# Performance work log

Hardware: AMD Instinct MI355X
Metric: run time of the kernel (lower is better)

The kernel has to match this reference:

```python
import jax, jax.numpy as jnp
import numpy as np

D = 64      # n_embd (== head_size in this module)
H = 8       # n_heads
B = 4
T = 2048    # seq len == block_size
EPS = 1e-5


def layernorm(x, g, b):
    mu = jnp.mean(x, axis=-1, keepdims=True)
    var = jnp.mean(jnp.square(x - mu), axis=-1, keepdims=True)
    return (x - mu) * jax.lax.rsqrt(var + EPS) * g + b


def setup_inputs() -> dict:
    key = jax.random.key(0)
    ks = jax.random.split(key, 16)
    s = 1.0 / np.sqrt(D)
    inp = {
        'inputs': jax.random.normal(ks[0], (B, T, D), jnp.float32),
        # per-head QKV linears: weight [H, D, D] (in, out), bias [H, D]
        'Wq': jax.random.uniform(ks[1], (H, D, D), jnp.float32, -s, s),
        'bq': jax.random.uniform(ks[2], (H, D), jnp.float32, -s, s),
        'Wk': jax.random.uniform(ks[3], (H, D, D), jnp.float32, -s, s),
        'bk': jax.random.uniform(ks[4], (H, D), jnp.float32, -s, s),
        'Wv': jax.random.uniform(ks[5], (H, D, D), jnp.float32, -s, s),
        'bv': jax.random.uniform(ks[6], (H, D), jnp.float32, -s, s),
        # projection: Linear(H*D -> D)
        'Wp': jax.random.uniform(ks[7], (H * D, D), jnp.float32, -1/np.sqrt(H*D), 1/np.sqrt(H*D)),
        'bp': jax.random.uniform(ks[8], (D,), jnp.float32, -1/np.sqrt(H*D), 1/np.sqrt(H*D)),
        # FFN: D -> 4D -> D
        'W1': jax.random.uniform(ks[9], (D, 4 * D), jnp.float32, -s, s),
        'b1': jax.random.uniform(ks[10], (4 * D,), jnp.float32, -s, s),
        'W2': jax.random.uniform(ks[11], (4 * D, D), jnp.float32, -1/np.sqrt(4*D), 1/np.sqrt(4*D)),
        'b2': jax.random.uniform(ks[12], (D,), jnp.float32, -1/np.sqrt(4*D), 1/np.sqrt(4*D)),
        'g1': jnp.ones((D,), jnp.float32), 'be1': jnp.zeros((D,), jnp.float32),
        'g2': jnp.ones((D,), jnp.float32), 'be2': jnp.zeros((D,), jnp.float32),
    }
    return inp


def reference(inputs, Wq, bq, Wk, bk, Wv, bv, Wp, bp, W1, b1, W2, b2, g1, be1, g2, be2):
    x = inputs
    # per-head full-width QKV: [H, B, T, D]
    q = jnp.einsum('btd,hde->hbte', x, Wq) + bq[:, None, None, :]
    k = jnp.einsum('btd,hde->hbte', x, Wk) + bk[:, None, None, :]
    v = jnp.einsum('btd,hde->hbte', x, Wv) + bv[:, None, None, :]
    # unscaled scores (module has no 1/sqrt(d) scaling)
    scores = jnp.einsum('hbte,hbse->hbts', q, k)  # [H, B, T, T]
    causal = jnp.tril(jnp.ones((T, T), bool))
    scores = jnp.where(causal, scores, -jnp.inf)
    attn = jax.nn.softmax(scores, axis=-1)
    out = jnp.einsum('hbts,hbse->hbte', attn, v)  # [H, B, T, D]
    # torch.cat over heads along last dim -> [B, T, H*D]
    cat = jnp.transpose(out, (1, 2, 0, 3)).reshape(B, T, H * D)
    attn_out = cat @ Wp + bp
    h1 = layernorm(x + attn_out, g1, be1)
    ffn = jax.nn.relu(h1 @ W1 + b1) @ W2 + b2
    return layernorm(h1 + ffn, g2, be2)
```

## Files before the change

### kernel.cpp

```cpp
#include <hip/hip_runtime.h>
#include <hip/hip_bf16.h>
#include <stdint.h>

#define Dd 64
#define Hh 8
#define Bb 4
#define Tt 2048
#define NT (Bb * Tt)

typedef __attribute__((ext_vector_type(4))) float f32x4;
typedef __attribute__((ext_vector_type(8))) __bf16 bf16x8;
typedef __attribute__((ext_vector_type(8))) uint16_t u16x8;
typedef __attribute__((ext_vector_type(4))) uint16_t u16x4;

__device__ __forceinline__ uint16_t f2bf_fast(float f) {
    union { __bf16 h; uint16_t u; } c; c.h = (__bf16)f; return c.u;
}
__device__ __forceinline__ uint32_t pkbf(float a, float b) {
    return (uint32_t)f2bf_fast(a) | ((uint32_t)f2bf_fast(b) << 16);
}

#define SWZ(row, k)   ((row) * 72  + ((k) ^ ((((row) >> 3) & 7) << 3)))
#define PSZ(q, k)     ((q)  * 72  + ((k) ^ ((((q)  >> 2) & 3) << 3)))
#define HSZ(q, k)     ((q)  * 264 + ((k) ^ ((((q)  >> 2) & 3) << 3)))
#define W2SWZ(col, k) ((col) * 264 + ((k) ^ ((((col) >> 3) & 7) << 3)))
#define WPSWZ(col, k) ((col) * 520 + ((k) ^ ((((col) >> 3) & 7) << 3)))

__global__ __launch_bounds__(256) void setup_kernel(
    const float* __restrict__ x,
    const float* __restrict__ Wq, const float* __restrict__ Wk,
    const float* __restrict__ Wv, const float* __restrict__ Wp,
    const float* __restrict__ W1, const float* __restrict__ W2,
    uint16_t* __restrict__ xb, uint16_t* __restrict__ WtAll,
    uint16_t* __restrict__ WptS, uint16_t* __restrict__ W1g,
    uint16_t* __restrict__ W2g)
{
    const int bid = blockIdx.x, t = threadIdx.x;
    if (bid < 256) {
        size_t base = ((size_t)bid * 256 + t) * 8;
        f32x4 a = *(const f32x4*)&x[base];
        f32x4 b = *(const f32x4*)&x[base + 4];
        u16x8 o;
#pragma unroll
        for (int j = 0; j < 4; ++j) { o[j] = f2bf_fast(a[j]); o[4 + j] = f2bf_fast(b[j]); }
        *(u16x8*)&xb[base] = o;
    } else if (bid < 280) {
        const int mh = bid - 256, m = mh / 8, h = mh % 8;
        const float* W = (m == 0) ? Wq : (m == 1) ? Wk : Wv;
        uint16_t* dst = WtAll + (size_t)mh * 4608;
#pragma unroll
        for (int p = 0; p < 4; ++p) {
            int idx = p * 256 + t;
            int k = idx >> 4, c4 = (idx & 15) * 4;
            f32x4 wv = *(const f32x4*)&W[(size_t)(h * 64 + k) * 64 + c4];
#pragma unroll
            for (int j = 0; j < 4; ++j) dst[SWZ(c4 + j, k)] = f2bf_fast(wv[j]);
        }
    } else if (bid < 288) {
        const int j = bid - 280;
#pragma unroll
        for (int p = 0; p < 16; ++p) {
            int idx = p * 256 + t;
            int col = idx & 63, k = j * 64 + (idx >> 6);
            WptS[WPSWZ(col, k)] = f2bf_fast(Wp[(size_t)k * 64 + col]);
        }
    } else if (bid < 292) {
        const int j = bid - 288;
#pragma unroll
        for (int p = 0; p < 16; ++p) {
            int e = j * 4096 + p * 256 + t;
            int col = e & 255, k = e >> 8;
            W1g[SWZ(col, k)] = f2bf_fast(W1[(size_t)k * 256 + col]);
        }
    } else {
        const int j = bid - 292;
#pragma unroll
        for (int p = 0; p < 16; ++p) {
            int e = j * 4096 + p * 256 + t;
            int col = e & 63, k = e >> 6;
            W2g[W2SWZ(col, k)] = f2bf_fast(W2[(size_t)k * 64 + col]);
        }
    }
}

__global__ __launch_bounds__(256) void qkv_kernel(
    const uint16_t* __restrict__ xb, const uint16_t* __restrict__ WtAll,
    const float* __restrict__ bq, const float* __restrict__ bk,
    const float* __restrict__ bv,
    uint16_t* __restrict__ qb, uint16_t* __restrict__ kb, uint16_t* __restrict__ vb)
{
    __shared__ uint16_t WtF[64 * 72];
    const int rt = blockIdx.x, h = blockIdx.y, m = blockIdx.z;
    const float* bias = (m == 0) ? bq : (m == 1) ? bk : bv;
    const int t = threadIdx.x, lane = t & 63, w = t >> 6;
    const int l15 = lane & 15, g = lane >> 4;

    {
        const u16x8* src = (const u16x8*)(WtAll + (size_t)(m * 8 + h) * 4608);
        u16x8* dst = (u16x8*)WtF;
        dst[t] = src[t];
        dst[256 + t] = src[256 + t];
        if (t < 64) dst[512 + t] = src[512 + t];
    }
    const int row = rt * 64 + w * 16 + l15;
    bf16x8 a0 = *(const bf16x8*)&xb[(size_t)row * 64 + g * 8];
    bf16x8 a1 = *(const bf16x8*)&xb[(size_t)row * 64 + 32 + g * 8];
    __syncthreads();

    f32x4 acc[4] = {};
#pragma unroll
    for (int ct = 0; ct < 4; ++ct) {
        bf16x8 b0 = *(const bf16x8*)&WtF[SWZ(ct * 16 + l15, g * 8)];
        bf16x8 b1 = *(const bf16x8*)&WtF[SWZ(ct * 16 + l15, 32 + g * 8)];
        acc[ct] = __builtin_amdgcn_mfma_f32_16x16x32_bf16(a0, b0, acc[ct], 0, 0, 0);
        acc[ct] = __builtin_amdgcn_mfma_f32_16x16x32_bf16(a1, b1, acc[ct], 0, 0, 0);
    }
    if (m < 2) {
        uint16_t* out = (m == 0) ? qb : kb;
#pragma unroll
        for (int ct = 0; ct < 4; ++ct) {
            float bb = bias[h * 64 + ct * 16 + l15];
#pragma unroll
            for (int rr = 0; rr < 4; ++rr) {
                int orow = rt * 64 + w * 16 + g * 4 + rr;
                out[((size_t)h * NT + orow) * 64 + ct * 16 + l15] =
                    f2bf_fast(acc[ct][rr] + bb);
            }
        }
    } else {
        const size_t tb = ((size_t)h * NT + (size_t)rt * 64) * 64;
#pragma unroll
        for (int ct = 0; ct < 4; ++ct) {
            float bb = bias[h * 64 + ct * 16 + l15];
            u16x4 vo;
#pragma unroll
            for (int rr = 0; rr < 4; ++rr) vo[rr] = f2bf_fast(acc[ct][rr] + bb);
            *(u16x4*)&vb[tb + (size_t)(ct * 16 + l15) * 64 + w * 16 + g * 4] = vo;
        }
    }
}

__global__ __launch_bounds__(128) void attn_kernel6(
    const uint16_t* __restrict__ qb, const uint16_t* __restrict__ kb,
    const uint16_t* __restrict__ vb, uint16_t* __restrict__ cat)
{
    __shared__ uint16_t KsF[2][64 * 72];
    __shared__ uint16_t VtF[2][64 * 72];
    const int bid = blockIdx.x;
    const int lbid = (bid & 7) * 128 + (bid >> 3);
    const int pairid = lbid & 31;
    const int hb = lbid >> 5;
    const int h = hb & 7, b = hb >> 3;
    const int t = threadIdx.x, lane = t & 63, w = t >> 6;
    const int l15 = lane & 15, g = lane >> 4;
    const size_t base = ((size_t)h * NT + (size_t)b * Tt) * 64;
    const uint16_t* Qh  = qb + base;
    const uint16_t* Kh  = kb + base;
    const uint16_t* VhT = vb + base;

    for (int ph = 0; ph < 2; ++ph) {
        const int qt32 = ph ? (63 - pairid) : pairid;
        bf16x8 aq0, aq1;
        {
            int qrow = qt32 * 32 + w * 16 + l15;
            aq0 = *(const bf16x8*)&Qh[(size_t)qrow * 64 + g * 8];
            aq1 = *(const bf16x8*)&Qh[(size_t)qrow * 64 + 32 + g * 8];
        }
        f32x4 o[4] = {};
        float m_run = -INFINITY, l_run = 0.f;

        __syncthreads();
#pragma unroll
        for (int i = 0; i < 4; ++i) {
            int slot = i * 128 + t;
            int r = slot >> 3, c8 = (slot & 7) * 8;
            size_t off = (size_t)r * 64 + c8;
            u16x8 kk = *(const u16x8*)&Kh[off];
            u16x8 vv = *(const u16x8*)&VhT[off];
            *(u16x8*)&KsF[0][SWZ(r, c8)] = kk;
            *(u16x8*)&VtF[0][SWZ(r, c8)] = vv;
        }
        __syncthreads();

        const int nkv = (qt32 >> 1) + 1;
        for (int kv = 0; kv < nkv; ++kv) {
            const int cur = kv & 1;
            const bool pf = (kv + 1) < nkv;
            u16x8 pK[4], pV[4];
            if (pf) {
                const size_t poff = (size_t)(kv + 1) * 4096;
#pragma unroll
                for (int i = 0; i < 4; ++i) {
                    int slot = i * 128 + t;
                    size_t off = poff + (size_t)(slot >> 3) * 64 + (slot & 7) * 8;
                    pK[i] = *(const u16x8*)&Kh[off];
                    pV[i] = *(const u16x8*)&VhT[off];
                }
            }
            f32x4 s[4];
#pragma unroll
            for (int kt = 0; kt < 4; ++kt) {
                bf16x8 bk0 = *(const bf16x8*)&KsF[cur][SWZ(kt * 16 + l15, g * 8)];
                bf16x8 bk1 = *(const bf16x8*)&KsF[cur][SWZ(kt * 16 + l15, 32 + g * 8)];
                f32x4 z = {};
                z = __builtin_amdgcn_mfma_f32_16x16x32_bf16(bk0, aq0, z, 0, 0, 0);
                z = __builtin_amdgcn_mfma_f32_16x16x32_bf16(bk1, aq1, z, 0, 0, 0);
                s[kt] = z;
            }
            if (kv == nkv - 1) {
                int qlocal = (qt32 & 1) * 32 + w * 16 + l15;
#pragma unroll
                for (int kt = 0; kt < 4; ++kt)
#pragma unroll
                    for (int rj = 0; rj < 4; ++rj)
                        if (kt * 16 + g * 4 + rj > qlocal) s[kt][rj] = -INFINITY;
            }
            float mt = s[0][0];
#pragma unroll
            for (int kt = 0; kt < 4; ++kt)
#pragma unroll
                for (int rj = 0; rj < 4; ++rj) mt = fmaxf(mt, s[kt][rj]);
            mt = fmaxf(mt, __shfl_xor(mt, 16));
            mt = fmaxf(mt, __shfl_xor(mt, 32));
            if (__any((int)(mt > m_run + 8.f))) {
                float mnew = fmaxf(m_run, mt);
                float alpha = __expf(m_run - mnew);
                m_run = mnew;
                l_run *= alpha;
                float a0 = __shfl(alpha, g * 4 + 0);
                float a1 = __shfl(alpha, g * 4 + 1);
                float a2 = __shfl(alpha, g * 4 + 2);
                float a3 = __shfl(alpha, g * 4 + 3);
#pragma unroll
                for (int dt = 0; dt < 4; ++dt) {
                    o[dt][0] *= a0; o[dt][1] *= a1; o[dt][2] *= a2; o[dt][3] *= a3;
                }
            }
            float ls = 0.f;
#pragma unroll
            for (int kt = 0; kt < 4; ++kt)
#pragma unroll
                for (int rj = 0; rj < 4; ++rj) {
                    float p = __expf(s[kt][rj] - m_run);
                    s[kt][rj] = p;
                    ls += p;
                }
            ls += __shfl_xor(ls, 16);
            ls += __shfl_xor(ls, 32);
            l_run += ls;
            union { uint32_t wd[4]; bf16x8 v; } ap0, ap1;
            ap0.wd[0] = pkbf(s[0][0], s[0][1]); ap0.wd[1] = pkbf(s[0][2], s[0][3]);
            ap0.wd[2] = pkbf(s[1][0], s[1][1]); ap0.wd[3] = pkbf(s[1][2], s[1][3]);
            ap1.wd[0] = pkbf(s[2][0], s[2][1]); ap1.wd[1] = pkbf(s[2][2], s[2][3]);
            ap1.wd[2] = pkbf(s[3][0], s[3][1]); ap1.wd[3] = pkbf(s[3][2], s[3][3]);
#pragma unroll
            for (int c = 0; c < 2; ++c) {
                const bf16x8 ap = c ? ap1.v : ap0.v;
#pragma unroll
                for (int dt = 0; dt < 4; ++dt) {
                    union { u16x4 q[2]; bf16x8 v; } bb;
                    bb.q[0] = *(const u16x4*)&VtF[cur][SWZ(dt * 16 + l15, c * 32 + g * 4)];
                    bb.q[1] = *(const u16x4*)&VtF[cur][SWZ(dt * 16 + l15, c * 32 + 16 + g * 4)];
                    o[dt] = __builtin_amdgcn_mfma_f32_16x16x32_bf16(ap, bb.v, o[dt], 0, 0, 0);
                }
            }
            if (pf) {
#pragma unroll
                for (int i = 0; i < 4; ++i) {
                    int slot = i * 128 + t;
                    int r = slot >> 3, c8 = (slot & 7) * 8;
                    *(u16x8*)&KsF[cur ^ 1][SWZ(r, c8)] = pK[i];
                    *(u16x8*)&VtF[cur ^ 1][SWZ(r, c8)] = pV[i];
                }
                __syncthreads();
            }
        }
        float inv = 1.f / l_run;
        float i0 = __shfl(inv, g * 4 + 0);
        float i1 = __shfl(inv, g * 4 + 1);
        float i2 = __shfl(inv, g * 4 + 2);
        float i3 = __shfl(inv, g * 4 + 3);
#pragma unroll
        for (int dt = 0; dt < 4; ++dt) {
            int rowb = qt32 * 32 + w * 16 + g * 4;
            size_t cb = ((size_t)b * Tt + rowb) * 512 + h * 64 + dt * 16 + l15;
            cat[cb]        = f2bf_fast(o[dt][0] * i0);
            cat[cb + 512]  = f2bf_fast(o[dt][1] * i1);
            cat[cb + 1024] = f2bf_fast(o[dt][2] * i2);
            cat[cb + 1536] = f2bf_fast(o[dt][3] * i3);
        }
    }
}

__global__ __launch_bounds__(128) void tail_kernel(
    const uint16_t* __restrict__ cat, const uint16_t* __restrict__ WptS,
    const uint16_t* __restrict__ W1g, const uint16_t* __restrict__ W2g,
    const float* __restrict__ bp, const float* __restrict__ b1,
    const float* __restrict__ b2, const float* __restrict__ x,
    const float* __restrict__ g1, const float* __restrict__ be1,
    const float* __restrict__ g2, const float* __restrict__ be2,
    float* __restrict__ out)
{
    __shared__ uint16_t h1S[2][16 * 72];
    __shared__ uint16_t hidS[2][16 * 264];
    const int rt = blockIdx.x;
    const int t = threadIdx.x, lane = t & 63, w = t >> 6;
    const int l15 = lane & 15, g = lane >> 4;
    const int arow = rt * 32 + w * 16 + l15;

    f32x4 acc[4] = {};
#pragma unroll
    for (int kt = 0; kt < 16; ++kt) {
        bf16x8 a = *(const bf16x8*)&cat[(size_t)arow * 512 + kt * 32 + g * 8];
#pragma unroll
        for (int ct = 0; ct < 4; ++ct) {
            bf16x8 bfr = *(const bf16x8*)&WptS[WPSWZ(ct * 16 + l15, kt * 32 + g * 8)];
            acc[ct] = __builtin_amdgcn_mfma_f32_16x16x32_bf16(a, bfr, acc[ct], 0, 0, 0);
        }
    }
    float bpv[4], g1v[4], b1v[4];
#pragma unroll
    for (int ct = 0; ct < 4; ++ct) {
        bpv[ct] = bp[ct * 16 + l15];
        g1v[ct] = g1[ct * 16 + l15];
        b1v[ct] = be1[ct * 16 + l15];
    }
    float hv[4][4];
#pragma unroll
    for (int rr = 0; rr < 4; ++rr) {
        int drow = rt * 32 + w * 16 + g * 4 + rr;
        float s[4], sum = 0.f;
#pragma unroll
        for (int ct = 0; ct < 4; ++ct) {
            s[ct] = acc[ct][rr] + bpv[ct] + x[(size_t)drow * 64 + ct * 16 + l15];
            sum += s[ct];
        }
        sum += __shfl_xor(sum, 1); sum += __shfl_xor(sum, 2);
        sum += __shfl_xor(sum, 4); sum += __shfl_xor(sum, 8);
        float mu = sum * (1.f / 64.f);
        float v = 0.f;
#pragma unroll
        for (int ct = 0; ct < 4; ++ct) { s[ct] -= mu; v += s[ct] * s[ct]; }
        v += __shfl_xor(v, 1); v += __shfl_xor(v, 2);
        v += __shfl_xor(v, 4); v += __shfl_xor(v, 8);
        float rstd = rsqrtf(v * (1.f / 64.f) + 1e-5f);
#pragma unroll
        for (int ct = 0; ct < 4; ++ct) {
            float h = s[ct] * rstd * g1v[ct] + b1v[ct];
            hv[ct][rr] = h;
            h1S[w][PSZ(g * 4 + rr, ct * 16 + l15)] = f2bf_fast(h);
        }
    }
    bf16x8 ha0 = *(const bf16x8*)&h1S[w][PSZ(l15, g * 8)];
    bf16x8 ha1 = *(const bf16x8*)&h1S[w][PSZ(l15, 32 + g * 8)];
#pragma unroll
    for (int nt = 0; nt < 16; ++nt) {
        f32x4 a1c = {};
        bf16x8 w10 = *(const bf16x8*)&W1g[SWZ(nt * 16 + l15, g * 8)];
        bf16x8 w11 = *(const bf16x8*)&W1g[SWZ(nt * 16 + l15, 32 + g * 8)];
        a1c = __builtin_amdgcn_mfma_f32_16x16x32_bf16(ha0, w10, a1c, 0, 0, 0);
        a1c = __builtin_amdgcn_mfma_f32_16x16x32_bf16(ha1, w11, a1c, 0, 0, 0);
        float bb1 = b1[nt * 16 + l15];
#pragma unroll
        for (int rr = 0; rr < 4; ++rr)
            hidS[w][HSZ(g * 4 + rr, nt * 16 + l15)] =
                f2bf_fast(fmaxf(a1c[rr] + bb1, 0.f));
    }
    f32x4 acc2[4] = {};
#pragma unroll
    for (int ks = 0; ks < 8; ++ks) {
        bf16x8 hfr = *(const bf16x8*)&hidS[w][HSZ(l15, ks * 32 + g * 8)];
#pragma unroll
        for (int ct = 0; ct < 4; ++ct) {
            bf16x8 w2f = *(const bf16x8*)&W2g[W2SWZ(ct * 16 + l15, ks * 32 + g * 8)];
            acc2[ct] = __builtin_amdgcn_mfma_f32_16x16x32_bf16(hfr, w2f, acc2[ct], 0, 0, 0);
        }
    }
    float b2v[4], g2v[4], be2v[4];
#pragma unroll
    for (int ct = 0; ct < 4; ++ct) {
        b2v[ct]  = b2[ct * 16 + l15];
        g2v[ct]  = g2[ct * 16 + l15];
        be2v[ct] = be2[ct * 16 + l15];
    }
#pragma unroll
    for (int rr = 0; rr < 4; ++rr) {
        int drow = rt * 32 + w * 16 + g * 4 + rr;
        float s[4], sum = 0.f;
#pragma unroll
        for (int ct = 0; ct < 4; ++ct) {
            s[ct] = acc2[ct][rr] + b2v[ct] + hv[ct][rr];
            sum += s[ct];
        }
        sum += __shfl_xor(sum, 1); sum += __shfl_xor(sum, 2);
        sum += __shfl_xor(sum, 4); sum += __shfl_xor(sum, 8);
        float mu = sum * (1.f / 64.f);
        float v = 0.f;
#pragma unroll
        for (int ct = 0; ct < 4; ++ct) { s[ct] -= mu; v += s[ct] * s[ct]; }
        v += __shfl_xor(v, 1); v += __shfl_xor(v, 2);
        v += __shfl_xor(v, 4); v += __shfl_xor(v, 8);
        float rstd = rsqrtf(v * (1.f / 64.f) + 1e-5f);
#pragma unroll
        for (int ct = 0; ct < 4; ++ct)
            out[(size_t)drow * 64 + ct * 16 + l15] =
                s[ct] * rstd * g2v[ct] + be2v[ct];
    }
}

extern "C" void kernel_launch(void* const* d_in, const int* in_sizes, int n_in,
                              void* d_out, int out_size, void* d_ws, size_t ws_size,
                              hipStream_t stream)
{
    (void)in_sizes; (void)n_in; (void)out_size; (void)ws_size;
    const float* x   = (const float*)d_in[0];
    const float* Wq  = (const float*)d_in[1];
    const float* bq  = (const float*)d_in[2];
    const float* Wk  = (const float*)d_in[3];
    const float* bk  = (const float*)d_in[4];
    const float* Wv  = (const float*)d_in[5];
    const float* bv  = (const float*)d_in[6];
    const float* Wp  = (const float*)d_in[7];
    const float* bp  = (const float*)d_in[8];
    const float* W1  = (const float*)d_in[9];
    const float* b1  = (const float*)d_in[10];
    const float* W2  = (const float*)d_in[11];
    const float* b2  = (const float*)d_in[12];
    const float* g1  = (const float*)d_in[13];
    const float* be1 = (const float*)d_in[14];
    const float* g2  = (const float*)d_in[15];
    const float* be2 = (const float*)d_in[16];
    float* outp = (float*)d_out;

    char* w = (char*)d_ws;
    uint16_t* qb   = (uint16_t*)w;
    uint16_t* kb   = qb + (size_t)Hh * NT * 64;
    uint16_t* vb   = kb + (size_t)Hh * NT * 64;
    uint16_t* cat  = vb + (size_t)Hh * NT * 64;
    uint16_t* WptS = cat + (size_t)NT * 512;
    uint16_t* W1g  = WptS + 33280;
    uint16_t* W2g  = W1g + 18432;
    uint16_t* xb   = W2g + 16896;
    uint16_t* WtAll= xb + (size_t)NT * 64;

    setup_kernel<<<dim3(296), dim3(256), 0, stream>>>(
        x, Wq, Wk, Wv, Wp, W1, W2, xb, WtAll, WptS, W1g, W2g);
    qkv_kernel<<<dim3(NT / 64, Hh, 3), dim3(256), 0, stream>>>(
        xb, WtAll, bq, bk, bv, qb, kb, vb);
    attn_kernel6<<<dim3(1024), dim3(128), 0, stream>>>(qb, kb, vb, cat);
    tail_kernel<<<dim3(256), dim3(128), 0, stream>>>(
        cat, WptS, W1g, W2g, bp, b1, b2, x, g1, be1, g2, be2, outp);
}
```

Measured before the change: 167.9 us.

## Fuse QKV projections per block and permute V layout for single-vector loads

The QKV kernel now computes Q, K and V in one block, loading all three weight tiles into shared memory and reusing the same x fragments instead of launching a third grid dimension. V is stored with a permuted key-column order so that the attention kernel can fetch each MFMA B operand with one 16-byte LDS read instead of two 8-byte reads. The row max in attention becomes a tree reduction. This trades more shared memory and serial work per QKV block for fewer redundant x loads and cheaper V reads in the hot attention loop.

```diff
diff --git a/kernel.cpp b/kernel.cpp
--- a/kernel.cpp
+++ b/kernel.cpp
@@ -89,15 +89,15 @@
     const float* __restrict__ bv,
     uint16_t* __restrict__ qb, uint16_t* __restrict__ kb, uint16_t* __restrict__ vb)
 {
-    __shared__ uint16_t WtF[64 * 72];
-    const int rt = blockIdx.x, h = blockIdx.y, m = blockIdx.z;
-    const float* bias = (m == 0) ? bq : (m == 1) ? bk : bv;
+    __shared__ uint16_t WtF[3][64 * 72];
+    const int rt = blockIdx.x, h = blockIdx.y;
     const int t = threadIdx.x, lane = t & 63, w = t >> 6;
     const int l15 = lane & 15, g = lane >> 4;
 
-    {
+#pragma unroll
+    for (int m = 0; m < 3; ++m) {
         const u16x8* src = (const u16x8*)(WtAll + (size_t)(m * 8 + h) * 4608);
-        u16x8* dst = (u16x8*)WtF;
+        u16x8* dst = (u16x8*)WtF[m];
         dst[t] = src[t];
         dst[256 + t] = src[256 + t];
         if (t < 64) dst[512 + t] = src[512 + t];
@@ -107,40 +107,45 @@
     bf16x8 a1 = *(const bf16x8*)&xb[(size_t)row * 64 + 32 + g * 8];
     __syncthreads();
 
-    f32x4 acc[4] = {};
-#pragma unroll
-    for (int ct = 0; ct < 4; ++ct) {
-        bf16x8 b0 = *(const bf16x8*)&WtF[SWZ(ct * 16 + l15, g * 8)];
-        bf16x8 b1 = *(const bf16x8*)&WtF[SWZ(ct * 16 + l15, 32 + g * 8)];
-        acc[ct] = __builtin_amdgcn_mfma_f32_16x16x32_bf16(a0, b0, acc[ct], 0, 0, 0);
-        acc[ct] = __builtin_amdgcn_mfma_f32_16x16x32_bf16(a1, b1, acc[ct], 0, 0, 0);
-    }
-    if (m < 2) {
-        uint16_t* out = (m == 0) ? qb : kb;
-#pragma unroll
-        for (int ct = 0; ct < 4; ++ct) {
-            float bb = bias[h * 64 + ct * 16 + l15];
-#pragma unroll
-            for (int rr = 0; rr < 4; ++rr) {
-                int orow = rt * 64 + w * 16 + g * 4 + rr;
-                out[((size_t)h * NT + orow) * 64 + ct * 16 + l15] =
-                    f2bf_fast(acc[ct][rr] + bb);
-            }
-        }
-    } else {
-        const size_t tb = ((size_t)h * NT + (size_t)rt * 64) * 64;
-#pragma unroll
-        for (int ct = 0; ct < 4; ++ct) {
-            float bb = bias[h * 64 + ct * 16 + l15];
-            u16x4 vo;
-#pragma unroll
-            for (int rr = 0; rr < 4; ++rr) vo[rr] = f2bf_fast(acc[ct][rr] + bb);
-            *(u16x4*)&vb[tb + (size_t)(ct * 16 + l15) * 64 + w * 16 + g * 4] = vo;
-        }
-    }
-}
-
-__global__ __launch_bounds__(128) void attn_kernel6(
+#pragma unroll
+    for (int m = 0; m < 3; ++m) {
+        const float* bias = (m == 0) ? bq : (m == 1) ? bk : bv;
+        f32x4 acc[4] = {};
+#pragma unroll
+        for (int ct = 0; ct < 4; ++ct) {
+            bf16x8 b0 = *(const bf16x8*)&WtF[m][SWZ(ct * 16 + l15, g * 8)];
+            bf16x8 b1 = *(const bf16x8*)&WtF[m][SWZ(ct * 16 + l15, 32 + g * 8)];
+            acc[ct] = __builtin_amdgcn_mfma_f32_16x16x32_bf16(a0, b0, acc[ct], 0, 0, 0);
+            acc[ct] = __builtin_amdgcn_mfma_f32_16x16x32_bf16(a1, b1, acc[ct], 0, 0, 0);
+        }
+        if (m < 2) {
+            uint16_t* out = (m == 0) ? qb : kb;
+#pragma unroll
+            for (int ct = 0; ct < 4; ++ct) {
+                float bb = bias[h * 64 + ct * 16 + l15];
+#pragma unroll
+                for (int rr = 0; rr < 4; ++rr) {
+                    int orow = rt * 64 + w * 16 + g * 4 + rr;
+                    out[((size_t)h * NT + orow) * 64 + ct * 16 + l15] =
+                        f2bf_fast(acc[ct][rr] + bb);
+                }
+            }
+        } else {
+            const size_t tb = ((size_t)h * NT + (size_t)rt * 64) * 64;
+            const int kcol = (w >> 1) * 32 + g * 8 + (w & 1) * 4;
+#pragma unroll
+            for (int ct = 0; ct < 4; ++ct) {
+                float bb = bias[h * 64 + ct * 16 + l15];
+                u16x4 vo;
+#pragma unroll
+                for (int rr = 0; rr < 4; ++rr) vo[rr] = f2bf_fast(acc[ct][rr] + bb);
+                *(u16x4*)&vb[tb + (size_t)(ct * 16 + l15) * 64 + kcol] = vo;
+            }
+        }
+    }
+}
+
+__global__ __launch_bounds__(128) void attn_kernel7(
     const uint16_t* __restrict__ qb, const uint16_t* __restrict__ kb,
     const uint16_t* __restrict__ vb, uint16_t* __restrict__ cat)
 {
@@ -215,11 +220,10 @@
                     for (int rj = 0; rj < 4; ++rj)
                         if (kt * 16 + g * 4 + rj > qlocal) s[kt][rj] = -INFINITY;
             }
-            float mt = s[0][0];
-#pragma unroll
-            for (int kt = 0; kt < 4; ++kt)
-#pragma unroll
-                for (int rj = 0; rj < 4; ++rj) mt = fmaxf(mt, s[kt][rj]);
+            float mt = fmaxf(fmaxf(fmaxf(s[0][0], s[0][1]), fmaxf(s[0][2], s[0][3])),
+                             fmaxf(fmaxf(s[1][0], s[1][1]), fmaxf(s[1][2], s[1][3])));
+            mt = fmaxf(mt, fmaxf(fmaxf(fmaxf(s[2][0], s[2][1]), fmaxf(s[2][2], s[2][3])),
+                                 fmaxf(fmaxf(s[3][0], s[3][1]), fmaxf(s[3][2], s[3][3]))));
             mt = fmaxf(mt, __shfl_xor(mt, 16));
             mt = fmaxf(mt, __shfl_xor(mt, 32));
             if (__any((int)(mt > m_run + 8.f))) {
@@ -258,10 +262,8 @@
                 const bf16x8 ap = c ? ap1.v : ap0.v;
 #pragma unroll
                 for (int dt = 0; dt < 4; ++dt) {
-                    union { u16x4 q[2]; bf16x8 v; } bb;
-                    bb.q[0] = *(const u16x4*)&VtF[cur][SWZ(dt * 16 + l15, c * 32 + g * 4)];
-                    bb.q[1] = *(const u16x4*)&VtF[cur][SWZ(dt * 16 + l15, c * 32 + 16 + g * 4)];
-                    o[dt] = __builtin_amdgcn_mfma_f32_16x16x32_bf16(ap, bb.v, o[dt], 0, 0, 0);
+                    bf16x8 bv = *(const bf16x8*)&VtF[cur][SWZ(dt * 16 + l15, c * 32 + g * 8)];
+                    o[dt] = __builtin_amdgcn_mfma_f32_16x16x32_bf16(ap, bv, o[dt], 0, 0, 0);
                 }
             }
             if (pf) {
@@ -445,9 +447,9 @@
 
     setup_kernel<<<dim3(296), dim3(256), 0, stream>>>(
         x, Wq, Wk, Wv, Wp, W1, W2, xb, WtAll, WptS, W1g, W2g);
-    qkv_kernel<<<dim3(NT / 64, Hh, 3), dim3(256), 0, stream>>>(
+    qkv_kernel<<<dim3(NT / 64, Hh), dim3(256), 0, stream>>>(
         xb, WtAll, bq, bk, bv, qb, kb, vb);
-    attn_kernel6<<<dim3(1024), dim3(128), 0, stream>>>(qb, kb, vb, cat);
+    attn_kernel7<<<dim3(1024), dim3(128), 0, stream>>>(qb, kb, vb, cat);
     tail_kernel<<<dim3(256), dim3(128), 0, stream>>>(
         cat, WptS, W1g, W2g, bp, b1, b2, x, g1, be1, g2, be2, outp);
 }
```

Measured after the change: 165.2 us. No clear change (-1.6%).
